# Kernel optimization log

Measured on AMD Instinct MI355X. Metric: run time of the kernel, lower is better.

The kernel has to match this reference:

```python
import jax, jax.numpy as jnp
import numpy as np

N, IN_CH, HID, N_CLS = 12000, 256, 64, 40
EDGE_PROB = 0.002  # ~24 avg degree


def setup_inputs() -> dict:
    key = jax.random.key(0)
    k = jax.random.split(key, 5)
    x = jax.random.normal(k[0], (N, IN_CH), dtype=jnp.float32)
    adj = (jax.random.uniform(k[1], (N, N), dtype=jnp.float32) < EDGE_PROB).astype(jnp.float32)
    W_in = jax.random.normal(k[2], (IN_CH, HID), dtype=jnp.float32) * 0.05
    b_in = jnp.zeros((HID,), dtype=jnp.float32)
    W_cls = jax.random.normal(k[3], (HID, N_CLS), dtype=jnp.float32) * 0.05
    b_cls = jnp.zeros((N_CLS,), dtype=jnp.float32)
    return {"x": x, "adj": adj, "W_in": W_in, "b_in": b_in, "W_cls": W_cls, "b_cls": b_cls}


def reference(x, adj, W_in, b_in, W_cls, b_cls):
    # fc_in projection (always applied in AllGNN.forward)
    h = x @ W_in + b_in                         # [N, HID]
    # calc_degree(adj).unsqueeze(-1): row-sum degree reduction
    deg = jnp.sum(adj, axis=1, keepdims=True)   # [N, 1]
    # degree-informed classifier: mean-style neighborhood aggregation + linear head
    agg = (adj @ h) / (deg + 1.0)               # [N, HID]
    out = agg @ W_cls + b_cls                   # [N, N_CLS]
    return out
```

## Files before the change

### kernel.cpp

```cpp
#include <hip/hip_runtime.h>


#define NN     12000
#define INCH   256
#define HID    64
#define NCLS   40
#define NCHUNK ((NN + 255) / 256)

typedef float f4 __attribute__((ext_vector_type(4)));

__global__ __launch_bounds__(256) void fc_in_kernel(
    const float* __restrict__ x, const float* __restrict__ W_in,
    const float* __restrict__ b_in, float* __restrict__ h)
{
    const int lane = threadIdx.x & 63;
    const int row  = blockIdx.x * 4 + (threadIdx.x >> 6);
    if (row >= NN) return;

    const float* xrow = x + (size_t)row * INCH;
    float xr0 = xrow[lane];
    float xr1 = xrow[64 + lane];
    float xr2 = xrow[128 + lane];
    float xr3 = xrow[192 + lane];

    float acc = b_in[lane];
    #pragma unroll 8
    for (int c = 0; c < 64; ++c) {
        float x0 = __shfl(xr0, c);
        float x1 = __shfl(xr1, c);
        float x2 = __shfl(xr2, c);
        float x3 = __shfl(xr3, c);
        acc = fmaf(x0, W_in[(c)       * HID + lane], acc);
        acc = fmaf(x1, W_in[(c + 64)  * HID + lane], acc);
        acc = fmaf(x2, W_in[(c + 128) * HID + lane], acc);
        acc = fmaf(x3, W_in[(c + 192) * HID + lane], acc);
    }
    h[(size_t)row * HID + lane] = acc;
}

__global__ __launch_bounds__(256) void gnn_agg_kernel(
    const float* __restrict__ adj, const float* __restrict__ h,
    const float* __restrict__ W_cls, const float* __restrict__ b_cls,
    float* __restrict__ out)
{
    const int lane = threadIdx.x & 63;
    const int w    = threadIdx.x >> 6;
    const int row  = blockIdx.x;

    __shared__ float s_acc[4][HID];
    __shared__ float s_deg[4];

    const float* __restrict__ arow = adj + (size_t)row * NN;
    const int bl = lane * 4;

    float acc = 0.0f;
    float deg = 0.0f;

    auto loadc = [&](int ci) -> f4 {
        const int base = ci * 256 + bl;
        f4 v = {0.f, 0.f, 0.f, 0.f};
        if (base + 4 <= NN)
            v = __builtin_nontemporal_load(reinterpret_cast<const f4*>(arow + base));
        return v;
    };

    auto process = [&](f4 v, int colbase) {
        float s = (v[0] + v[1]) + (v[2] + v[3]);
        deg += s;
        unsigned long long m = __ballot(s != 0.0f);
        while (m) {
            int l = (int)__builtin_ctzll(m); m &= m - 1;
            int col = colbase + l * 4;
            float a0 = __shfl(v[0], l);
            float a1 = __shfl(v[1], l);
            float a2 = __shfl(v[2], l);
            float a3 = __shfl(v[3], l);
            const float* hc = h + (size_t)col * HID + lane;
            if (a0 != 0.0f) acc = fmaf(a0, hc[0 * HID], acc);
            if (a1 != 0.0f) acc = fmaf(a1, hc[1 * HID], acc);
            if (a2 != 0.0f) acc = fmaf(a2, hc[2 * HID], acc);
            if (a3 != 0.0f) acc = fmaf(a3, hc[3 * HID], acc);
        }
    };

    f4 v0 = loadc(w);
    f4 v1 = (w + 4 < NCHUNK) ? loadc(w + 4) : f4{0.f, 0.f, 0.f, 0.f};
    for (int c = w; c < NCHUNK; c += 8) {
        f4 p0 = {0.f, 0.f, 0.f, 0.f}, p1 = {0.f, 0.f, 0.f, 0.f};
        if (c + 8  < NCHUNK) p0 = loadc(c + 8);
        if (c + 12 < NCHUNK) p1 = loadc(c + 12);
        process(v0, c * 256);
        process(v1, (c + 4) * 256);
        v0 = p0; v1 = p1;
    }

    #pragma unroll
    for (int off = 32; off; off >>= 1) deg += __shfl_xor(deg, off);
    s_acc[w][lane] = acc;
    if (lane == 0) s_deg[w] = deg;
    __syncthreads();

    if (w == 0) {
        float a  = (s_acc[0][lane] + s_acc[1][lane])
                 + (s_acc[2][lane] + s_acc[3][lane]);
        float dt = (s_deg[0] + s_deg[1]) + (s_deg[2] + s_deg[3]);
        float agg = a * __frcp_rn(dt + 1.0f);

        const int cl = (lane < NCLS) ? lane : 0;
        float o = b_cls[cl];
        #pragma unroll 8
        for (int k = 0; k < HID; ++k) {
            float av = __shfl(agg, k);
            o = fmaf(av, W_cls[k * NCLS + cl], o);
        }
        if (lane < NCLS) out[(size_t)row * NCLS + lane] = o;
    }
}

extern "C" void kernel_launch(void* const* d_in, const int* in_sizes, int n_in,
                              void* d_out, int out_size, void* d_ws, size_t ws_size,
                              hipStream_t stream)
{
    const float* x     = (const float*)d_in[0];
    const float* adj   = (const float*)d_in[1];
    const float* W_in  = (const float*)d_in[2];
    const float* b_in  = (const float*)d_in[3];
    const float* W_cls = (const float*)d_in[4];
    const float* b_cls = (const float*)d_in[5];
    float* out = (float*)d_out;
    float* h   = (float*)d_ws;

    fc_in_kernel<<<(NN + 3) / 4, 256, 0, stream>>>(x, W_in, b_in, h);
    gnn_agg_kernel<<<NN, 256, 0, stream>>>(adj, h, W_cls, b_cls, out);
}
```

Baseline: 143.3 us.

## Compact nonzeros into shared lists before gathering h; 4-row fc_in blocking

The aggregation kernel now scans adjacency rows and appends nonzero column/value pairs into per-wave shared-memory lists with LDS atomics. It then gathers h rows in batches of four independent loads, instead of serialising ballot/shuffle loops that interleave with the streaming loads. The adjacency loop now issues four chunk loads per iteration. fc_in computes four rows per wave with wave-uniform x loads, so each W_in element is reused four times. The risks are that lists are capped at 512 entries per wave, silently dropping edges beyond that, and that the result depends on NN being divisible by 16.

```diff
diff --git a/kernel.cpp b/kernel.cpp
--- a/kernel.cpp
+++ b/kernel.cpp
@@ -6,6 +6,7 @@
 #define HID    64
 #define NCLS   40
 #define NCHUNK ((NN + 255) / 256)
+#define CAP    512
 
 typedef float f4 __attribute__((ext_vector_type(4)));
 
@@ -14,28 +15,27 @@
     const float* __restrict__ b_in, float* __restrict__ h)
 {
     const int lane = threadIdx.x & 63;
-    const int row  = blockIdx.x * 4 + (threadIdx.x >> 6);
-    if (row >= NN) return;
+    const int w    = threadIdx.x >> 6;
+    int rbase = (blockIdx.x * 4 + w) * 4;
+    rbase = __builtin_amdgcn_readfirstlane(rbase);
 
-    const float* xrow = x + (size_t)row * INCH;
-    float xr0 = xrow[lane];
-    float xr1 = xrow[64 + lane];
-    float xr2 = xrow[128 + lane];
-    float xr3 = xrow[192 + lane];
+    const float* __restrict__ xr = x + (size_t)rbase * INCH;
+    const float  b = b_in[lane];
+    float acc0 = b, acc1 = b, acc2 = b, acc3 = b;
 
-    float acc = b_in[lane];
     #pragma unroll 8
-    for (int c = 0; c < 64; ++c) {
-        float x0 = __shfl(xr0, c);
-        float x1 = __shfl(xr1, c);
-        float x2 = __shfl(xr2, c);
-        float x3 = __shfl(xr3, c);
-        acc = fmaf(x0, W_in[(c)       * HID + lane], acc);
-        acc = fmaf(x1, W_in[(c + 64)  * HID + lane], acc);
-        acc = fmaf(x2, W_in[(c + 128) * HID + lane], acc);
-        acc = fmaf(x3, W_in[(c + 192) * HID + lane], acc);
+    for (int c = 0; c < INCH; ++c) {
+        float wv = W_in[c * HID + lane];
+        acc0 = fmaf(xr[c],            wv, acc0);
+        acc1 = fmaf(xr[INCH + c],     wv, acc1);
+        acc2 = fmaf(xr[2 * INCH + c], wv, acc2);
+        acc3 = fmaf(xr[3 * INCH + c], wv, acc3);
     }
-    h[(size_t)row * HID + lane] = acc;
+    float* hp = h + (size_t)rbase * HID + lane;
+    hp[0 * HID] = acc0;
+    hp[1 * HID] = acc1;
+    hp[2 * HID] = acc2;
+    hp[3 * HID] = acc3;
 }
 
 __global__ __launch_bounds__(256) void gnn_agg_kernel(
@@ -47,13 +47,16 @@
     const int w    = threadIdx.x >> 6;
     const int row  = blockIdx.x;
 
+    __shared__ int   s_cnt[4];
+    __shared__ int   s_col[4][CAP];
+    __shared__ float s_val[4][CAP];
     __shared__ float s_acc[4][HID];
     __shared__ float s_deg[4];
 
+    if (lane == 0) s_cnt[w] = 0;
+
     const float* __restrict__ arow = adj + (size_t)row * NN;
     const int bl = lane * 4;
-
-    float acc = 0.0f;
     float deg = 0.0f;
 
     auto loadc = [&](int ci) -> f4 {
@@ -63,36 +66,46 @@
             v = __builtin_nontemporal_load(reinterpret_cast<const f4*>(arow + base));
         return v;
     };
-
-    auto process = [&](f4 v, int colbase) {
-        float s = (v[0] + v[1]) + (v[2] + v[3]);
-        deg += s;
-        unsigned long long m = __ballot(s != 0.0f);
-        while (m) {
-            int l = (int)__builtin_ctzll(m); m &= m - 1;
-            int col = colbase + l * 4;
-            float a0 = __shfl(v[0], l);
-            float a1 = __shfl(v[1], l);
-            float a2 = __shfl(v[2], l);
-            float a3 = __shfl(v[3], l);
-            const float* hc = h + (size_t)col * HID + lane;
-            if (a0 != 0.0f) acc = fmaf(a0, hc[0 * HID], acc);
-            if (a1 != 0.0f) acc = fmaf(a1, hc[1 * HID], acc);
-            if (a2 != 0.0f) acc = fmaf(a2, hc[2 * HID], acc);
-            if (a3 != 0.0f) acc = fmaf(a3, hc[3 * HID], acc);
+    auto scan = [&](f4 v, int ci) {
+        deg += (v[0] + v[1]) + (v[2] + v[3]);
+        const int col = ci * 256 + bl;
+        #pragma unroll
+        for (int i = 0; i < 4; ++i) {
+            if (v[i] != 0.0f) {
+                int idx = atomicAdd(&s_cnt[w], 1);
+                if (idx < CAP) { s_col[w][idx] = col + i; s_val[w][idx] = v[i]; }
+            }
         }
     };
 
-    f4 v0 = loadc(w);
-    f4 v1 = (w + 4 < NCHUNK) ? loadc(w + 4) : f4{0.f, 0.f, 0.f, 0.f};
-    for (int c = w; c < NCHUNK; c += 8) {
-        f4 p0 = {0.f, 0.f, 0.f, 0.f}, p1 = {0.f, 0.f, 0.f, 0.f};
-        if (c + 8  < NCHUNK) p0 = loadc(c + 8);
-        if (c + 12 < NCHUNK) p1 = loadc(c + 12);
-        process(v0, c * 256);
-        process(v1, (c + 4) * 256);
-        v0 = p0; v1 = p1;
+    for (int c = w; c < NCHUNK; c += 16) {
+        f4 v0 = loadc(c);
+        f4 v1 = (c + 4  < NCHUNK) ? loadc(c + 4)  : f4{0.f, 0.f, 0.f, 0.f};
+        f4 v2 = (c + 8  < NCHUNK) ? loadc(c + 8)  : f4{0.f, 0.f, 0.f, 0.f};
+        f4 v3 = (c + 12 < NCHUNK) ? loadc(c + 12) : f4{0.f, 0.f, 0.f, 0.f};
+        scan(v0, c);
+        scan(v1, c + 4);
+        scan(v2, c + 8);
+        scan(v3, c + 12);
     }
+
+    float acc = 0.0f;
+    int n = s_cnt[w];
+    n = (n < CAP) ? n : CAP;
+    int i = 0;
+    for (; i + 4 <= n; i += 4) {
+        int   c0 = s_col[w][i],     c1 = s_col[w][i + 1];
+        int   c2 = s_col[w][i + 2], c3 = s_col[w][i + 3];
+        float a0 = s_val[w][i],     a1 = s_val[w][i + 1];
+        float a2 = s_val[w][i + 2], a3 = s_val[w][i + 3];
+        float h0 = h[(size_t)c0 * HID + lane];
+        float h1 = h[(size_t)c1 * HID + lane];
+        float h2 = h[(size_t)c2 * HID + lane];
+        float h3 = h[(size_t)c3 * HID + lane];
+        acc = fmaf(a0, h0, fmaf(a1, h1, fmaf(a2, h2, fmaf(a3, h3, acc))));
+    }
+    for (; i < n; ++i)
+        acc = fmaf(s_val[w][i], h[(size_t)s_col[w][i] * HID + lane], acc);
 
     #pragma unroll
     for (int off = 32; off; off >>= 1) deg += __shfl_xor(deg, off);
@@ -130,6 +143,6 @@
     float* out = (float*)d_out;
     float* h   = (float*)d_ws;
 
-    fc_in_kernel<<<(NN + 3) / 4, 256, 0, stream>>>(x, W_in, b_in, h);
+    fc_in_kernel<<<NN / 16, 256, 0, stream>>>(x, W_in, b_in, h);
     gnn_agg_kernel<<<NN, 256, 0, stream>>>(adj, h, W_cls, b_cls, out);
 }
```

Measured after the change: 114.9 us. 19.8% less time.
